# Optimization experiments

Hardware: AMD Instinct MI355X
Metric: run time of the kernel (lower is better)

Reference implementation:

```python
import jax, jax.numpy as jnp
import numpy as np

IRE = 1.0 / 400.0

def _stencil(f):
    # f: [B, C, X, Y]; returns (u,v) 5-point stencil fields, each [B, X-2, Y-2]
    m = f[:, :, 1:-1, 1:-1]
    l = f[:, :, :-2, 1:-1]
    r = f[:, :, 2:, 1:-1]
    b = f[:, :, 1:-1, :-2]
    t = f[:, :, 1:-1, 2:]
    return (m[:, 0], m[:, 1], l[:, 0], l[:, 1], r[:, 0], r[:, 1],
            b[:, 0], b[:, 1], t[:, 0], t[:, 1])

def _residuals(um, vm, ul, vl, ur, vr, ub, vb, ut, vt):
    dudx = (ur - ul) * 0.5
    dvdy = (vt - vb) * 0.5
    dudy = (ut - ub) * 0.5
    dvdx = (vr - vl) * 0.5
    du2dx = 0.25 * ((ur + um) ** 2 - (ul + um) ** 2)
    duvdy = 0.25 * ((ut + um) * (vt + vm) - (ub + um) * (vb + vm))
    dv2dy = 0.25 * ((vt + vm) ** 2 - (vb + vm) ** 2)
    dvudx = 0.25 * ((vr + vm) * (ur + um) - (vl + vm) * (ul + um))
    dudx2 = ur - um * 2 + ul
    dudy2 = ut - um * 2 + ub
    dvdx2 = vr - vm * 2 + vl
    dvdy2 = vt - vm * 2 + vb
    mass = dudx + dvdy
    mom_u = du2dx + duvdy - (dudx2 + dudy2) * IRE
    mom_v = dvudx + dv2dy - (dvdx2 + dvdy2) * IRE
    return mass, mom_u, mom_v, dudx, dudy, dvdx, dvdy

def setup_inputs() -> dict:
    key = jax.random.key(0)
    k1, k2 = jax.random.split(key)
    pred = jax.random.normal(k1, (64, 2, 512, 512), dtype=jnp.float32)
    trut = jax.random.normal(k2, (64, 2, 512, 512), dtype=jnp.float32)
    return {"pred": pred, "trut": trut}

def reference(pred, trut):
    mass_t, momu_t, momv_t, dudx_t, dudy_t, dvdx_t, dvdy_t = _residuals(*_stencil(trut))
    mass_p, momu_p, momv_p, dudx_p, dudy_p, dvdx_p, dvdy_p = _residuals(*_stencil(pred))
    lossMass = jnp.mean(jnp.abs(mass_t - mass_p))
    lossMom = jnp.mean(jnp.abs(momu_t - momu_p) + jnp.abs(momv_t - momv_p))
    lossGdl = jnp.mean(jnp.abs(dudx_t - dudx_p) + jnp.abs(dudy_t - dudy_p)
                       + jnp.abs(dvdx_t - dvdx_p) + jnp.abs(dvdy_t - dvdy_p)) / 4.0
    lossL1 = jnp.mean(jnp.abs(pred - trut))
    # lossGdl computed (as in original) but unused in the final combination
    del lossGdl
    return (lossMass * 5 + lossMom * 25 + lossL1) / 3
```

## Files before the change

kernel.cpp:

```cpp
#include <hip/hip_runtime.h>

#define IRE (1.0f / 400.0f)

constexpr int W = 512;
constexpr int H = 512;
constexpr int NB = 64;
constexpr int ROWS = 8;
constexpr int CHUNKS = H / ROWS;
constexpr int STRIPS = 2;
constexpr int NWAVES = NB * CHUNKS * STRIPS;
constexpr int WPB = 4;
constexpr int GRID = NWAVES / WPB;

struct RowT  { float4 tu, tv, pu, pv; };
struct EdgeT { float tu, tv, pu, pv; };

__device__ __forceinline__ void residuals3(
    float um, float vm, float ul, float vl, float ur, float vr,
    float ub, float vb, float ut, float vt,
    float& mass, float& momu, float& momv)
{
    float dudx = (ur - ul) * 0.5f;
    float dvdy = (vt - vb) * 0.5f;
    float ru = ur + um, lu = ul + um, tu_ = ut + um, bu = ub + um;
    float rv = vr + vm, lv = vl + vm, tv_ = vt + vm, bv = vb + vm;
    float du2dx = 0.25f * (ru * ru - lu * lu);
    float duvdy = 0.25f * (tu_ * tv_ - bu * bv);
    float dv2dy = 0.25f * (tv_ * tv_ - bv * bv);
    float dvudx = 0.25f * (rv * ru - lv * lu);
    float dudx2 = ur - 2.0f * um + ul;
    float dudy2 = ut - 2.0f * um + ub;
    float dvdx2 = vr - 2.0f * vm + vl;
    float dvdy2 = vt - 2.0f * vm + vb;
    mass = dudx + dvdy;
    momu = du2dx + duvdy - (dudx2 + dudy2) * IRE;
    momv = dvudx + dv2dy - (dvdx2 + dvdy2) * IRE;
}

__global__ __launch_bounds__(256) void loss_main(
    const float* __restrict__ pred, const float* __restrict__ trut,
    double* __restrict__ partial)
{
    const int tid  = (int)threadIdx.x;
    const int lane = tid & 63;
    const int gw    = (int)blockIdx.x * WPB + (tid >> 6);
    const int strip = gw % STRIPS;
    const int chunk = (gw / STRIPS) % CHUNKS;
    const int b     = gw / (STRIPS * CHUNKS);

    const int r0 = chunk * ROWS;
    const int js = strip * 256 + lane * 4;
    const int colE = (strip == 0) ? 256 : 255;

    const size_t CH = (size_t)H * W;
    const float* g_tu = trut + (size_t)b * 2 * CH;
    const float* g_tv = g_tu + CH;
    const float* g_pu = pred + (size_t)b * 2 * CH;
    const float* g_pv = g_pu + CH;

    float accMass = 0.0f, accMom = 0.0f, accL1 = 0.0f;

    RowT  ring[5];
    EdgeT ering[3];

    auto clampr = [](int r) { return r < 0 ? 0 : (r > H - 1 ? H - 1 : r); };
    auto loadRow = [&](int r, RowT& R) {
        const size_t off = (size_t)r * W + js;
        R.tu = *(const float4*)(g_tu + off);
        R.tv = *(const float4*)(g_tv + off);
        R.pu = *(const float4*)(g_pu + off);
        R.pv = *(const float4*)(g_pv + off);
    };
    auto loadEdge = [&](int r, EdgeT& E) {
        const size_t o = (size_t)r * W + colE;
        E.tu = g_tu[o]; E.tv = g_tv[o]; E.pu = g_pu[o]; E.pv = g_pv[o];
    };
    auto l1row = [&](const RowT& R) {
        accL1 += fabsf(R.pu.x - R.tu.x) + fabsf(R.pu.y - R.tu.y)
               + fabsf(R.pu.z - R.tu.z) + fabsf(R.pu.w - R.tu.w)
               + fabsf(R.pv.x - R.tv.x) + fabsf(R.pv.y - R.tv.y)
               + fabsf(R.pv.z - R.tv.z) + fabsf(R.pv.w - R.tv.w);
    };

    loadRow(clampr(r0 - 1), ring[0]);
    loadRow(r0,             ring[1]);
    loadRow(r0 + 1,         ring[2]);
    loadRow(r0 + 2,         ring[3]);
    loadEdge(r0,     ering[0]);
    loadEdge(r0 + 1, ering[1]);

    #pragma unroll
    for (int s = 0; s < ROWS; ++s) {
        if (s <= 5) loadRow(clampr(r0 + s + 3), ring[(s + 4) % 5]);
        if (s <= 5) loadEdge(r0 + s + 2, ering[(s + 2) % 3]);

        const RowT& Pr = ring[s % 5];
        const RowT& Xr = ring[(s + 1) % 5];
        const RowT& Nr = ring[(s + 2) % 5];

        l1row(Xr);

        const int r = r0 + s;
        if (r >= 1 && r <= H - 2) {
            const EdgeT& E = ering[s % 3];

            float Ltu = __shfl_up(Xr.tu.w, 1), Rtu = __shfl_down(Xr.tu.x, 1);
            float Ltv = __shfl_up(Xr.tv.w, 1), Rtv = __shfl_down(Xr.tv.x, 1);
            float Lpu = __shfl_up(Xr.pu.w, 1), Rpu = __shfl_down(Xr.pu.x, 1);
            float Lpv = __shfl_up(Xr.pv.w, 1), Rpv = __shfl_down(Xr.pv.x, 1);
            if (lane == 0)  { Ltu = E.tu; Ltv = E.tv; Lpu = E.pu; Lpv = E.pv; }
            if (lane == 63) { Rtu = E.tu; Rtv = E.tv; Rpu = E.pu; Rpv = E.pv; }

            const float ctu[6] = {Ltu, Xr.tu.x, Xr.tu.y, Xr.tu.z, Xr.tu.w, Rtu};
            const float ctv[6] = {Ltv, Xr.tv.x, Xr.tv.y, Xr.tv.z, Xr.tv.w, Rtv};
            const float cpu_[6]= {Lpu, Xr.pu.x, Xr.pu.y, Xr.pu.z, Xr.pu.w, Rpu};
            const float cpv[6] = {Lpv, Xr.pv.x, Xr.pv.y, Xr.pv.z, Xr.pv.w, Rpv};
            const float ptu[4] = {Pr.tu.x, Pr.tu.y, Pr.tu.z, Pr.tu.w};
            const float ptv[4] = {Pr.tv.x, Pr.tv.y, Pr.tv.z, Pr.tv.w};
            const float ppu[4] = {Pr.pu.x, Pr.pu.y, Pr.pu.z, Pr.pu.w};
            const float ppv[4] = {Pr.pv.x, Pr.pv.y, Pr.pv.z, Pr.pv.w};
            const float ntu[4] = {Nr.tu.x, Nr.tu.y, Nr.tu.z, Nr.tu.w};
            const float ntv[4] = {Nr.tv.x, Nr.tv.y, Nr.tv.z, Nr.tv.w};
            const float npu[4] = {Nr.pu.x, Nr.pu.y, Nr.pu.z, Nr.pu.w};
            const float npv[4] = {Nr.pv.x, Nr.pv.y, Nr.pv.z, Nr.pv.w};

            #pragma unroll
            for (int k = 0; k < 4; ++k) {
                const int j = js + k;
                if (j >= 1 && j <= W - 2) {
                    float mT, uT, vT, mP, uP, vP;
                    residuals3(ctu[k+1], ctv[k+1], ptu[k], ptv[k], ntu[k], ntv[k],
                               ctu[k],   ctv[k],   ctu[k+2], ctv[k+2], mT, uT, vT);
                    residuals3(cpu_[k+1], cpv[k+1], ppu[k], ppv[k], npu[k], npv[k],
                               cpu_[k],   cpv[k],   cpu_[k+2], cpv[k+2], mP, uP, vP);
                    accMass += fabsf(mT - mP);
                    accMom  += fabsf(uT - uP) + fabsf(vT - vP);
                }
            }
        }
    }

    float res = 5.0f * accMass + 25.0f * accMom;
    float l1  = accL1;
    #pragma unroll
    for (int off = 32; off > 0; off >>= 1) {
        res += __shfl_down(res, off);
        l1  += __shfl_down(l1, off);
    }
    if (lane == 0) {
        partial[(size_t)gw * 2 + 0] = (double)res;
        partial[(size_t)gw * 2 + 1] = (double)l1;
    }
}

__global__ __launch_bounds__(256) void loss_final(
    const double* __restrict__ partial, float* __restrict__ out)
{
    __shared__ double sres[4], sl1[4];
    const int t = threadIdx.x;
    double res = 0.0, l1 = 0.0;
    for (int i = t; i < NWAVES; i += 256) {
        res += partial[(size_t)i * 2 + 0];
        l1  += partial[(size_t)i * 2 + 1];
    }
    #pragma unroll
    for (int off = 32; off > 0; off >>= 1) {
        res += __shfl_down(res, off);
        l1  += __shfl_down(l1, off);
    }
    const int wave = t >> 6;
    if ((t & 63) == 0) { sres[wave] = res; sl1[wave] = l1; }
    __syncthreads();
    if (t == 0) {
        res = sres[0] + sres[1] + sres[2] + sres[3];
        l1  = sl1[0] + sl1[1] + sl1[2] + sl1[3];
        const double nRes = 64.0 * 510.0 * 510.0;
        const double nL1  = 64.0 * 2.0 * 512.0 * 512.0;
        out[0] = (float)((res / nRes + l1 / nL1) / 3.0);
    }
}

extern "C" void kernel_launch(void* const* d_in, const int* in_sizes, int n_in,
                              void* d_out, int out_size, void* d_ws, size_t ws_size,
                              hipStream_t stream)
{
    const float* pred = (const float*)d_in[0];
    const float* trut = (const float*)d_in[1];
    double* partial = (double*)d_ws;
    loss_main<<<GRID, 256, 0, stream>>>(pred, trut, partial);
    loss_final<<<1, 256, 0, stream>>>(partial, (float*)d_out);
}
```

Measured before the change: 286.8 us.

## Stream row tiles into LDS ring via direct global-to-LDS loads

Replaces per-wave register row rings with shuffle-based halos by block-level 32-row tiles staged into a five-slot shared-memory ring using direct global-to-LDS loads. Each wave loads one channel row, and all threads compute two columns from LDS neighbors, which removes edge loads and shuffles and cuts halo row reloads. Partial sums are reduced per block, giving fewer partials. A barrier per row and only one row of prefetch may limit memory overlap.

```diff
diff --git a/kernel.cpp b/kernel.cpp
--- a/kernel.cpp
+++ b/kernel.cpp
@@ -2,18 +2,14 @@
 
 #define IRE (1.0f / 400.0f)
 
-constexpr int W = 512;
-constexpr int H = 512;
+constexpr int W  = 512;
+constexpr int H  = 512;
 constexpr int NB = 64;
-constexpr int ROWS = 8;
-constexpr int CHUNKS = H / ROWS;
-constexpr int STRIPS = 2;
-constexpr int NWAVES = NB * CHUNKS * STRIPS;
-constexpr int WPB = 4;
-constexpr int GRID = NWAVES / WPB;
+constexpr int TR = 32;
+constexpr int TILES = H / TR;
+constexpr int NBLK  = NB * TILES;
+constexpr int NSLOT = 5;
 
-struct RowT  { float4 tu, tv, pu, pv; };
-struct EdgeT { float tu, tv, pu, pv; };
 
 __device__ __forceinline__ void residuals3(
     float um, float vm, float ul, float vl, float ur, float vr,
@@ -37,107 +33,96 @@
     momv = dvudx + dv2dy - (dvdx2 + dvdy2) * IRE;
 }
 
-__global__ __launch_bounds__(256) void loss_main(
+struct W8 { float c0, c1, lf, rt, u0, u1, d0, d1; };
+
+__global__ __launch_bounds__(256, 4) void loss_main(
     const float* __restrict__ pred, const float* __restrict__ trut,
     double* __restrict__ partial)
 {
+    __shared__ __align__(16) float ring[NSLOT * 4 * W];
+
     const int tid  = (int)threadIdx.x;
     const int lane = tid & 63;
-    const int gw    = (int)blockIdx.x * WPB + (tid >> 6);
-    const int strip = gw % STRIPS;
-    const int chunk = (gw / STRIPS) % CHUNKS;
-    const int b     = gw / (STRIPS * CHUNKS);
-
-    const int r0 = chunk * ROWS;
-    const int js = strip * 256 + lane * 4;
-    const int colE = (strip == 0) ? 256 : 255;
+    const int wv   = tid >> 6;
+    const int blk  = (int)blockIdx.x;
+    const int tile = blk % TILES;
+    const int b    = blk / TILES;
+    const int r0   = tile * TR;
 
     const size_t CH = (size_t)H * W;
-    const float* g_tu = trut + (size_t)b * 2 * CH;
-    const float* g_tv = g_tu + CH;
-    const float* g_pu = pred + (size_t)b * 2 * CH;
-    const float* g_pv = g_pu + CH;
+    const float* gbase = (wv < 2 ? trut : pred) + (size_t)b * 2 * CH + (size_t)(wv & 1) * CH;
+
+    auto stage_row = [&](int row, int slot) {
+        row = row < 0 ? 0 : (row > H - 1 ? H - 1 : row);
+        const float* src = gbase + (size_t)row * W + lane * 4;
+        float* dst = &ring[(slot * 4 + wv) * W];
+        __builtin_amdgcn_global_load_lds(
+            (const __attribute__((address_space(1))) void*)src,
+            (__attribute__((address_space(3))) void*)dst, 16, 0, 0);
+        __builtin_amdgcn_global_load_lds(
+            (const __attribute__((address_space(1))) void*)(src + 256),
+            (__attribute__((address_space(3))) void*)(dst + 256), 16, 0, 0);
+    };
+
+    stage_row(r0 - 1, 0);
+    stage_row(r0,     1);
+    stage_row(r0 + 1, 2);
+
+    const int j0  = tid * 2;
+    const int jm1 = (j0 == 0) ? 0 : j0 - 1;
+    const int jp2 = (j0 + 2 > W - 1) ? W - 1 : j0 + 2;
 
     float accMass = 0.0f, accMom = 0.0f, accL1 = 0.0f;
 
-    RowT  ring[5];
-    EdgeT ering[3];
+    int sTop = 0;
+    for (int s = 0; s < TR; ++s) {
+        const int r = r0 + s;
+        if (s < TR - 1) {
+            int sSt = sTop + 3; if (sSt >= NSLOT) sSt -= NSLOT;
+            stage_row(r + 2, sSt);
+            asm volatile("s_waitcnt vmcnt(2) lgkmcnt(0)\n\ts_barrier" ::: "memory");
+        } else {
+            asm volatile("s_waitcnt vmcnt(0) lgkmcnt(0)\n\ts_barrier" ::: "memory");
+        }
 
-    auto clampr = [](int r) { return r < 0 ? 0 : (r > H - 1 ? H - 1 : r); };
-    auto loadRow = [&](int r, RowT& R) {
-        const size_t off = (size_t)r * W + js;
-        R.tu = *(const float4*)(g_tu + off);
-        R.tv = *(const float4*)(g_tv + off);
-        R.pu = *(const float4*)(g_pu + off);
-        R.pv = *(const float4*)(g_pv + off);
-    };
-    auto loadEdge = [&](int r, EdgeT& E) {
-        const size_t o = (size_t)r * W + colE;
-        E.tu = g_tu[o]; E.tv = g_tv[o]; E.pu = g_pu[o]; E.pv = g_pv[o];
-    };
-    auto l1row = [&](const RowT& R) {
-        accL1 += fabsf(R.pu.x - R.tu.x) + fabsf(R.pu.y - R.tu.y)
-               + fabsf(R.pu.z - R.tu.z) + fabsf(R.pu.w - R.tu.w)
-               + fabsf(R.pv.x - R.tv.x) + fabsf(R.pv.y - R.tv.y)
-               + fabsf(R.pv.z - R.tv.z) + fabsf(R.pv.w - R.tv.w);
-    };
+        int sMid = sTop + 1; if (sMid >= NSLOT) sMid -= NSLOT;
+        int sBot = sMid + 1; if (sBot >= NSLOT) sBot -= NSLOT;
+        const float* top = &ring[sTop * 4 * W];
+        const float* mid = &ring[sMid * 4 * W];
+        const float* bot = &ring[sBot * 4 * W];
 
-    loadRow(clampr(r0 - 1), ring[0]);
-    loadRow(r0,             ring[1]);
-    loadRow(r0 + 1,         ring[2]);
-    loadRow(r0 + 2,         ring[3]);
-    loadEdge(r0,     ering[0]);
-    loadEdge(r0 + 1, ering[1]);
+        W8 wtu, wtv, wpu, wpv;
+        #define LOADA(dst, a) \
+            dst.c0 = mid[(a)*W + j0]; dst.c1 = mid[(a)*W + j0 + 1]; \
+            dst.lf = mid[(a)*W + jm1]; dst.rt = mid[(a)*W + jp2]; \
+            dst.u0 = top[(a)*W + j0]; dst.u1 = top[(a)*W + j0 + 1]; \
+            dst.d0 = bot[(a)*W + j0]; dst.d1 = bot[(a)*W + j0 + 1];
+        LOADA(wtu, 0) LOADA(wtv, 1) LOADA(wpu, 2) LOADA(wpv, 3)
+        #undef LOADA
 
-    #pragma unroll
-    for (int s = 0; s < ROWS; ++s) {
-        if (s <= 5) loadRow(clampr(r0 + s + 3), ring[(s + 4) % 5]);
-        if (s <= 5) loadEdge(r0 + s + 2, ering[(s + 2) % 3]);
+        accL1 += fabsf(wpu.c0 - wtu.c0) + fabsf(wpu.c1 - wtu.c1)
+               + fabsf(wpv.c0 - wtv.c0) + fabsf(wpv.c1 - wtv.c1);
 
-        const RowT& Pr = ring[s % 5];
-        const RowT& Xr = ring[(s + 1) % 5];
-        const RowT& Nr = ring[(s + 2) % 5];
-
-        l1row(Xr);
-
-        const int r = r0 + s;
         if (r >= 1 && r <= H - 2) {
-            const EdgeT& E = ering[s % 3];
-
-            float Ltu = __shfl_up(Xr.tu.w, 1), Rtu = __shfl_down(Xr.tu.x, 1);
-            float Ltv = __shfl_up(Xr.tv.w, 1), Rtv = __shfl_down(Xr.tv.x, 1);
-            float Lpu = __shfl_up(Xr.pu.w, 1), Rpu = __shfl_down(Xr.pu.x, 1);
-            float Lpv = __shfl_up(Xr.pv.w, 1), Rpv = __shfl_down(Xr.pv.x, 1);
-            if (lane == 0)  { Ltu = E.tu; Ltv = E.tv; Lpu = E.pu; Lpv = E.pv; }
-            if (lane == 63) { Rtu = E.tu; Rtv = E.tv; Rpu = E.pu; Rpv = E.pv; }
-
-            const float ctu[6] = {Ltu, Xr.tu.x, Xr.tu.y, Xr.tu.z, Xr.tu.w, Rtu};
-            const float ctv[6] = {Ltv, Xr.tv.x, Xr.tv.y, Xr.tv.z, Xr.tv.w, Rtv};
-            const float cpu_[6]= {Lpu, Xr.pu.x, Xr.pu.y, Xr.pu.z, Xr.pu.w, Rpu};
-            const float cpv[6] = {Lpv, Xr.pv.x, Xr.pv.y, Xr.pv.z, Xr.pv.w, Rpv};
-            const float ptu[4] = {Pr.tu.x, Pr.tu.y, Pr.tu.z, Pr.tu.w};
-            const float ptv[4] = {Pr.tv.x, Pr.tv.y, Pr.tv.z, Pr.tv.w};
-            const float ppu[4] = {Pr.pu.x, Pr.pu.y, Pr.pu.z, Pr.pu.w};
-            const float ppv[4] = {Pr.pv.x, Pr.pv.y, Pr.pv.z, Pr.pv.w};
-            const float ntu[4] = {Nr.tu.x, Nr.tu.y, Nr.tu.z, Nr.tu.w};
-            const float ntv[4] = {Nr.tv.x, Nr.tv.y, Nr.tv.z, Nr.tv.w};
-            const float npu[4] = {Nr.pu.x, Nr.pu.y, Nr.pu.z, Nr.pu.w};
-            const float npv[4] = {Nr.pv.x, Nr.pv.y, Nr.pv.z, Nr.pv.w};
-
-            #pragma unroll
-            for (int k = 0; k < 4; ++k) {
-                const int j = js + k;
-                if (j >= 1 && j <= W - 2) {
-                    float mT, uT, vT, mP, uP, vP;
-                    residuals3(ctu[k+1], ctv[k+1], ptu[k], ptv[k], ntu[k], ntv[k],
-                               ctu[k],   ctv[k],   ctu[k+2], ctv[k+2], mT, uT, vT);
-                    residuals3(cpu_[k+1], cpv[k+1], ppu[k], ppv[k], npu[k], npv[k],
-                               cpu_[k],   cpv[k],   cpu_[k+2], cpv[k+2], mP, uP, vP);
-                    accMass += fabsf(mT - mP);
-                    accMom  += fabsf(uT - uP) + fabsf(vT - vP);
-                }
+            float mT, uT, vT, mP, uP, vP;
+            residuals3(wtu.c0, wtv.c0, wtu.u0, wtv.u0, wtu.d0, wtv.d0,
+                       wtu.lf, wtv.lf, wtu.c1, wtv.c1, mT, uT, vT);
+            residuals3(wpu.c0, wpv.c0, wpu.u0, wpv.u0, wpu.d0, wpv.d0,
+                       wpu.lf, wpv.lf, wpu.c1, wpv.c1, mP, uP, vP);
+            if (j0 >= 1) {
+                accMass += fabsf(mT - mP);
+                accMom  += fabsf(uT - uP) + fabsf(vT - vP);
+            }
+            residuals3(wtu.c1, wtv.c1, wtu.u1, wtv.u1, wtu.d1, wtv.d1,
+                       wtu.c0, wtv.c0, wtu.rt, wtv.rt, mT, uT, vT);
+            residuals3(wpu.c1, wpv.c1, wpu.u1, wpv.u1, wpu.d1, wpv.d1,
+                       wpu.c0, wpv.c0, wpu.rt, wpv.rt, mP, uP, vP);
+            if (j0 + 1 <= W - 2) {
+                accMass += fabsf(mT - mP);
+                accMom  += fabsf(uT - uP) + fabsf(vT - vP);
             }
         }
+        sTop = sMid;
     }
 
     float res = 5.0f * accMass + 25.0f * accMom;
@@ -147,9 +132,13 @@
         res += __shfl_down(res, off);
         l1  += __shfl_down(l1, off);
     }
-    if (lane == 0) {
-        partial[(size_t)gw * 2 + 0] = (double)res;
-        partial[(size_t)gw * 2 + 1] = (double)l1;
+    __syncthreads();
+    double* sred = (double*)ring;
+    if (lane == 0) { sred[wv] = (double)res; sred[4 + wv] = (double)l1; }
+    __syncthreads();
+    if (tid == 0) {
+        partial[(size_t)blk * 2 + 0] = sred[0] + sred[1] + sred[2] + sred[3];
+        partial[(size_t)blk * 2 + 1] = sred[4] + sred[5] + sred[6] + sred[7];
     }
 }
 
@@ -157,9 +146,9 @@
     const double* __restrict__ partial, float* __restrict__ out)
 {
     __shared__ double sres[4], sl1[4];
-    const int t = threadIdx.x;
+    const int t = (int)threadIdx.x;
     double res = 0.0, l1 = 0.0;
-    for (int i = t; i < NWAVES; i += 256) {
+    for (int i = t; i < NBLK; i += 256) {
         res += partial[(size_t)i * 2 + 0];
         l1  += partial[(size_t)i * 2 + 1];
     }
@@ -187,6 +176,6 @@
     const float* pred = (const float*)d_in[0];
     const float* trut = (const float*)d_in[1];
     double* partial = (double*)d_ws;
-    loss_main<<<GRID, 256, 0, stream>>>(pred, trut, partial);
+    loss_main<<<NBLK, 256, 0, stream>>>(pred, trut, partial);
     loss_final<<<1, 256, 0, stream>>>(partial, (float*)d_out);
 }
```

Measured after the change: 288.7 us. No clear change (+0.6%).
